# Kernel optimization log

Measured on AMD Instinct MI355X. Metric: run time of the kernel, lower is better.

The kernel has to match this reference:

```python
import jax, jax.numpy as jnp
import numpy as np

S, B, IN, OUT = 16, 32, 1024, 1024


def setup_inputs() -> dict:
    key = jax.random.key(0)
    ks = jax.random.split(key, 7)
    return {
        "input": jax.random.normal(ks[0], (S, B, IN), dtype=jnp.float32),
        "w_mu": jax.random.normal(ks[1], (OUT, IN), dtype=jnp.float32) * 0.1 - 3.0,
        "w_std_eta": jax.random.uniform(ks[2], (OUT, IN), dtype=jnp.float32, minval=-4.0, maxval=-2.0),
        "b_mu": jax.random.normal(ks[3], (OUT,), dtype=jnp.float32) * 0.03,
        "b_std_eta": jax.random.uniform(ks[4], (OUT,), dtype=jnp.float32, minval=-0.03, maxval=0.03),
        "eps_w": jax.random.normal(ks[5], (B, OUT, IN), dtype=jnp.float32),
        "eps_b": jax.random.normal(ks[6], (B, OUT), dtype=jnp.float32),
    }


def _kl_to_std_normal(mu, std):
    # KL( N(mu, std) || N(0, 1) ) elementwise, summed
    return jnp.sum(-jnp.log(std) + 0.5 * (std * std + mu * mu) - 0.5)


def reference(input, w_mu, w_std_eta, b_mu, b_std_eta, eps_w, eps_b):
    std_w = 1e-06 + jax.nn.softplus(w_std_eta)          # [OUT, IN]
    std_b = 1e-06 + jax.nn.softplus(b_std_eta)          # [OUT]
    # per-batch-element reparameterized positive weights: [B, OUT, IN]
    w = jnp.exp(w_mu[None, :, :] + std_w[None, :, :] * eps_w)
    b = b_mu[None, :] + std_b[None, :] * eps_b          # [B, OUT]
    # batched linear: for each b-index i: input[:, i, :] @ w[i].T + b[i]
    out = jnp.einsum('sbi,boi->sbo', input, w) + b[None, :, :]  # [S, B, OUT]
    kl_w = _kl_to_std_normal(w_mu, std_w)
    kl_b = _kl_to_std_normal(b_mu, std_b)
    return (out, kl_w, kl_b)
```

## Files before the change

kernel.cpp:

```cpp
#include <hip/hip_runtime.h>


constexpr int S_ = 16, B_ = 32, IN_ = 1024, OUT_ = 1024;

typedef __bf16 bf16x8 __attribute__((ext_vector_type(8)));
typedef float  f32x4  __attribute__((ext_vector_type(4)));

__device__ __forceinline__ float softplus_f(float x) {
    float e = __expf(-fabsf(x));
    return fmaxf(x, 0.0f) + __logf(1.0f + e);
}

__device__ __forceinline__ unsigned bf16_hi(float x) {
    return (__float_as_uint(x) + 0x8000u) & 0xffff0000u;
}

__global__ __launch_bounds__(256) void bpl_pre2(
    const float* __restrict__ input,
    const float* __restrict__ w_mu, const float* __restrict__ w_eta,
    unsigned* __restrict__ tbl_f,
    __bf16* __restrict__ a_ws,
    float* __restrict__ klw_part)
{
    const int tid = threadIdx.x;

    if (blockIdx.x >= 1024) {
        const int b = blockIdx.x - 1024;
        #pragma unroll
        for (int j = 0; j < 8; ++j) {
            const int c  = tid + j * 256;
            const int k0 = ((c >> 6) << 5) | (((c >> 4) & 3) << 3);
            const int s  = c & 15;
            const float* src = input + ((size_t)s * B_ + b) * IN_ + k0;
            const float4 x0 = *reinterpret_cast<const float4*>(src);
            const float4 x1 = *reinterpret_cast<const float4*>(src + 4);
            bf16x8 v;
            v[0] = (__bf16)x0.x; v[1] = (__bf16)x0.y; v[2] = (__bf16)x0.z; v[3] = (__bf16)x0.w;
            v[4] = (__bf16)x1.x; v[5] = (__bf16)x1.y; v[6] = (__bf16)x1.z; v[7] = (__bf16)x1.w;
            *reinterpret_cast<bf16x8*>(&a_ws[(size_t)b * 16384 + (size_t)c * 8]) = v;
        }
        return;
    }

    __shared__ float red[4];
    const int wid  = tid >> 6;
    const int lane = tid & 63;
    const int o    = blockIdx.x;
    const int ot   = o >> 4;
    const int on   = o & 15;

    const size_t base = (size_t)o * IN_ + tid * 4;
    const float4 mu = *reinterpret_cast<const float4*>(&w_mu[base]);
    const float4 et = *reinterpret_cast<const float4*>(&w_eta[base]);
    const float m[4] = {mu.x, mu.y, mu.z, mu.w};
    const float e[4] = {et.x, et.y, et.z, et.w};

    float local = 0.0f;
    #pragma unroll
    for (int j = 0; j < 4; ++j) {
        const int   i   = tid * 4 + j;
        const float sp  = __logf(1.0f + __expf(e[j])) + 1e-6f;
        const float spl = sp * 1.44269504f;
        const float emu = __expf(m[j]);
        const unsigned pk = bf16_hi(emu) | (bf16_hi(spl) >> 16);
        const int kt  = i >> 5;
        const int kg0 = (i >> 3) & 3;
        const int jj  = i & 7;
        const int ln  = kg0 * 16 + on;
        tbl_f[(((size_t)ot * 32 + kt) * 64 + ln) * 8 + jj] = pk;
        local += -__logf(sp) + 0.5f * fmaf(sp, sp, m[j] * m[j]) - 0.5f;
    }

    #pragma unroll
    for (int off = 32; off > 0; off >>= 1) local += __shfl_xor(local, off, 64);
    if (lane == 0) red[wid] = local;
    __syncthreads();
    if (tid == 0) klw_part[blockIdx.x] = red[0] + red[1] + red[2] + red[3];
}

__global__ __launch_bounds__(512, 4) void bpl_fused(
    const unsigned* __restrict__ tbl_f,
    const __bf16* __restrict__ a_ws,
    const float* __restrict__ eps_w,
    const float* __restrict__ b_mu,
    const float* __restrict__ b_eta,
    const float* __restrict__ eps_b,
    const float* __restrict__ klw_part,
    float* __restrict__ out,
    float* __restrict__ kl)
{
    const int blk = blockIdx.x;
    const int tid = threadIdx.x;

    if (blk == 2048) {
        __shared__ float kred[16];
        const int wid  = tid >> 6;
        const int lane = tid & 63;
        float lw = klw_part[tid] + klw_part[tid + 512];
        float lb;
        {
            const int o = tid;
            const float sd0 = softplus_f(b_eta[o]) + 1e-6f;
            const float m0  = b_mu[o];
            const float sd1 = softplus_f(b_eta[o + 512]) + 1e-6f;
            const float m1  = b_mu[o + 512];
            lb = (-__logf(sd0) + 0.5f * fmaf(sd0, sd0, m0 * m0) - 0.5f)
               + (-__logf(sd1) + 0.5f * fmaf(sd1, sd1, m1 * m1) - 0.5f);
        }
        #pragma unroll
        for (int off = 32; off > 0; off >>= 1) {
            lw += __shfl_xor(lw, off, 64);
            lb += __shfl_xor(lb, off, 64);
        }
        if (lane == 0) { kred[wid] = lw; kred[8 + wid] = lb; }
        __syncthreads();
        if (tid == 0) {
            float tw = 0.0f, tb = 0.0f;
            #pragma unroll
            for (int k = 0; k < 8; ++k) { tw += kred[k]; tb += kred[8 + k]; }
            kl[0] = tw; kl[1] = tb;
        }
        return;
    }

    __shared__ __align__(16) float smem[16384];

    const int xcd = blk & 7;
    const int r_  = blk >> 3;
    const int b   = r_ & 31;
    const int otl = r_ >> 5;
    const int o_base = xcd * 128 + otl * 16;
    const int ot_g   = o_base >> 4;

    const int kq   = tid >> 6;
    const int lane = tid & 63;
    const int on   = lane & 15;
    const int kg0  = lane >> 4;

    const float* eps_base = eps_w + ((size_t)(b * 1024 + o_base)) * 1024 + kq * 128;
    const int rlo = lane >> 5;
    const int cq  = lane & 31;
    float4 ev[8];
    #pragma unroll
    for (int j = 0; j < 8; ++j) {
        const int r = 2 * j + rlo;
        ev[j] = *reinterpret_cast<const float4*>(eps_base + (size_t)r * 1024 + cq * 4);
    }

    const unsigned* tf = tbl_f + (((size_t)ot_g * 32 + kq * 4) * 64 + lane) * 8;
    uint4 t0[4], t1[4];
    #pragma unroll
    for (int t = 0; t < 4; ++t) {
        t0[t] = *reinterpret_cast<const uint4*>(tf + t * 512);
        t1[t] = *reinterpret_cast<const uint4*>(tf + t * 512 + 4);
    }

    const __bf16* ap = a_ws + (size_t)b * 16384 + (size_t)(kq * 4) * 512 + lane * 8;
    bf16x8 av[4];
    #pragma unroll
    for (int t = 0; t < 4; ++t)
        av[t] = *reinterpret_cast<const bf16x8*>(ap + t * 512);

    char* wbase = (char*)(smem + kq * 2048);
    #pragma unroll
    for (int j = 0; j < 8; ++j) {
        const int r    = 2 * j + rlo;
        const int byte = (cq * 16) ^ ((r & 7) << 4);
        *reinterpret_cast<float4*>(wbase + r * 512 + byte) = ev[j];
    }

    f32x4 acc = {0.0f, 0.0f, 0.0f, 0.0f};
    const int sw = (on & 7) << 4;
    #pragma unroll
    for (int t = 0; t < 4; ++t) {
        const f32x4 e0 = *reinterpret_cast<const f32x4*>(
            wbase + on * 512 + ((t * 128 + kg0 * 32) ^ sw));
        const f32x4 e1 = *reinterpret_cast<const f32x4*>(
            wbase + on * 512 + ((t * 128 + kg0 * 32 + 16) ^ sw));

        const unsigned uu[8] = {t0[t].x, t0[t].y, t0[t].z, t0[t].w,
                                t1[t].x, t1[t].y, t1[t].z, t1[t].w};
        const float    ee[8] = {e0[0], e0[1], e0[2], e0[3], e1[0], e1[1], e1[2], e1[3]};

        bf16x8 bfrag;
        #pragma unroll
        for (int q = 0; q < 8; ++q) {
            const float emu = __uint_as_float(uu[q] & 0xffff0000u);
            const float spl = __uint_as_float(uu[q] << 16);
            bfrag[q] = (__bf16)(emu * exp2f(spl * ee[q]));
        }
        acc = __builtin_amdgcn_mfma_f32_16x16x32_bf16(av[t], bfrag, acc, 0, 0, 0);
    }

    *reinterpret_cast<f32x4*>(&smem[kq * 2048 + lane * 4]) = acc;
    __syncthreads();

    if (tid < 256) {
        const int s  = tid >> 4;
        const int ol = tid & 15;
        const int srcLane = ((s >> 2) << 4) | ol;
        const int rr = s & 3;
        float v = 0.0f;
        #pragma unroll
        for (int k8 = 0; k8 < 8; ++k8)
            v += smem[k8 * 2048 + srcLane * 4 + rr];
        const int oo = o_base + ol;
        const float bias = fmaf(softplus_f(b_eta[oo]) + 1e-6f,
                                eps_b[(size_t)b * OUT_ + oo], b_mu[oo]);
        out[((size_t)s * B_ + b) * OUT_ + oo] = v + bias;
    }
}

__global__ __launch_bounds__(256) void bpl_pre_fb(
    const float* __restrict__ w_mu, const float* __restrict__ w_eta,
    const float* __restrict__ b_mu, const float* __restrict__ b_eta,
    float* __restrict__ kl)
{
    __shared__ float red[4];
    const int tid  = threadIdx.x;
    const int wid  = tid >> 6;
    const int lane = tid & 63;

    const size_t base = (size_t)blockIdx.x * IN_ + tid * 4;
    const float4 mu = *reinterpret_cast<const float4*>(&w_mu[base]);
    const float4 et = *reinterpret_cast<const float4*>(&w_eta[base]);
    const float m[4] = {mu.x, mu.y, mu.z, mu.w};
    const float e[4] = {et.x, et.y, et.z, et.w};

    float local = 0.0f;
    #pragma unroll
    for (int j = 0; j < 4; ++j) {
        const float sp = __logf(1.0f + __expf(e[j])) + 1e-6f;
        local += -__logf(sp) + 0.5f * fmaf(sp, sp, m[j] * m[j]) - 0.5f;
    }
    #pragma unroll
    for (int off = 32; off > 0; off >>= 1) local += __shfl_xor(local, off, 64);
    if (lane == 0) red[wid] = local;
    __syncthreads();
    if (tid == 0) atomicAdd(&kl[0], red[0] + red[1] + red[2] + red[3]);

    if (blockIdx.x != 0) return;
    float lb = 0.0f;
    #pragma unroll
    for (int j = 0; j < 4; ++j) {
        const int idx = tid * 4 + j;
        const float sd = softplus_f(b_eta[idx]) + 1e-6f;
        const float mm = b_mu[idx];
        lb += -__logf(sd) + 0.5f * fmaf(sd, sd, mm * mm) - 0.5f;
    }
    #pragma unroll
    for (int off = 32; off > 0; off >>= 1) lb += __shfl_xor(lb, off, 64);
    __syncthreads();
    if (lane == 0) red[wid] = lb;
    __syncthreads();
    if (tid == 0) atomicAdd(&kl[1], red[0] + red[1] + red[2] + red[3]);
}

__global__ __launch_bounds__(256, 4) void bpl_mfma_fb(
    const float* __restrict__ input, const float* __restrict__ w_mu,
    const float* __restrict__ w_eta, const float* __restrict__ b_mu,
    const float* __restrict__ b_eta, const float* __restrict__ eps_w,
    const float* __restrict__ eps_b, float* __restrict__ out)
{
    __shared__ __align__(16) __bf16 alds[16384];

    const int blk = blockIdx.x;
    const int xcd = blk & 7;
    const int r_  = blk >> 3;
    const int b   = r_ & 31;
    const int oh  = r_ >> 5;
    const int o_base = (xcd * 2 + oh) * 64;

    const int tid  = threadIdx.x;
    const int wid  = tid >> 6;
    const int lane = tid & 63;

    #pragma unroll
    for (int j = 0; j < 8; ++j) {
        const int c   = tid + j * 256;
        const int s   = c & 15;
        const int kgg = ((c >> 6) << 2) | ((c >> 4) & 3);
        const float* src = input + ((size_t)s * B_ + b) * IN_ + kgg * 8;
        const float4 x0 = *reinterpret_cast<const float4*>(src);
        const float4 x1 = *reinterpret_cast<const float4*>(src + 4);
        bf16x8 v;
        v[0] = (__bf16)x0.x; v[1] = (__bf16)x0.y; v[2] = (__bf16)x0.z; v[3] = (__bf16)x0.w;
        v[4] = (__bf16)x1.x; v[5] = (__bf16)x1.y; v[6] = (__bf16)x1.z; v[7] = (__bf16)x1.w;
        *reinterpret_cast<bf16x8*>(&alds[c * 8]) = v;
    }
    __syncthreads();

    const int on    = lane & 15;
    const int kg0   = lane >> 4;
    const int o_row = o_base + wid * 16 + on;

    const float* __restrict__ mu_p = w_mu  + (size_t)o_row * IN_ + kg0 * 8;
    const float* __restrict__ et_p = w_eta + (size_t)o_row * IN_ + kg0 * 8;
    const float* __restrict__ ep_p = eps_w + ((size_t)b * OUT_ + o_row) * IN_ + kg0 * 8;
    const __bf16* __restrict__ a_p = alds + lane * 8;

    f32x4 acc = {0.0f, 0.0f, 0.0f, 0.0f};
    #pragma unroll
    for (int kt = 0; kt < 32; ++kt) {
        const int i_ = kt * 32;
        const float4 m0 = *reinterpret_cast<const float4*>(mu_p + i_);
        const float4 m1 = *reinterpret_cast<const float4*>(mu_p + i_ + 4);
        const float4 s0 = *reinterpret_cast<const float4*>(et_p + i_);
        const float4 s1 = *reinterpret_cast<const float4*>(et_p + i_ + 4);
        const float4 e0 = *reinterpret_cast<const float4*>(ep_p + i_);
        const float4 e1 = *reinterpret_cast<const float4*>(ep_p + i_ + 4);
        const float mm[8] = {m0.x, m0.y, m0.z, m0.w, m1.x, m1.y, m1.z, m1.w};
        const float ss[8] = {s0.x, s0.y, s0.z, s0.w, s1.x, s1.y, s1.z, s1.w};
        const float ee[8] = {e0.x, e0.y, e0.z, e0.w, e1.x, e1.y, e1.z, e1.w};
        bf16x8 bfrag;
        #pragma unroll
        for (int q = 0; q < 8; ++q) {
            const float sp_ = __logf(1.0f + __expf(ss[q])) + 1e-6f;
            bfrag[q] = (__bf16)__expf(fmaf(sp_, ee[q], mm[q]));
        }
        const bf16x8 afrag = *reinterpret_cast<const bf16x8*>(a_p + kt * 512);
        acc = __builtin_amdgcn_mfma_f32_16x16x32_bf16(afrag, bfrag, acc, 0, 0, 0);
    }

    const float bias = fmaf(softplus_f(b_eta[o_row]) + 1e-6f,
                            eps_b[(size_t)b * OUT_ + o_row], b_mu[o_row]);
    #pragma unroll
    for (int rr = 0; rr < 4; ++rr) {
        const int s = kg0 * 4 + rr;
        out[((size_t)s * B_ + b) * OUT_ + o_row] = acc[rr] + bias;
    }
}

extern "C" void kernel_launch(void* const* d_in, const int* in_sizes, int n_in,
                              void* d_out, int out_size, void* d_ws, size_t ws_size,
                              hipStream_t stream)
{
    const float* input = (const float*)d_in[0];
    const float* w_mu  = (const float*)d_in[1];
    const float* w_eta = (const float*)d_in[2];
    const float* b_mu  = (const float*)d_in[3];
    const float* b_eta = (const float*)d_in[4];
    const float* eps_w = (const float*)d_in[5];
    const float* eps_b = (const float*)d_in[6];

    float* out = (float*)d_out;
    float* kl  = out + (size_t)S_ * B_ * OUT_;

    const size_t TBL_OFF = 0;
    const size_t A_OFF   = (size_t)4 * 1024 * 1024;
    const size_t KLP_OFF = (size_t)5 * 1024 * 1024;
    const size_t NEED    = KLP_OFF + 4096;

    if (ws_size >= NEED) {
        unsigned* tbl  = (unsigned*)((char*)d_ws + TBL_OFF);
        __bf16*   a_ws = (__bf16*)((char*)d_ws + A_OFF);
        float*    klp  = (float*)((char*)d_ws + KLP_OFF);

        bpl_pre2<<<1056, 256, 0, stream>>>(input, w_mu, w_eta, tbl, a_ws, klp);
        bpl_fused<<<2049, 512, 0, stream>>>(tbl, a_ws, eps_w, b_mu, b_eta, eps_b,
                                            klp, out, kl);
    } else {
        hipMemsetAsync(kl, 0, 2 * sizeof(float), stream);
        bpl_pre_fb<<<1024, 256, 0, stream>>>(w_mu, w_eta, b_mu, b_eta, kl);
        bpl_mfma_fb<<<512, 256, 0, stream>>>(input, w_mu, w_eta, b_mu, b_eta,
                                             eps_w, eps_b, out);
    }
}
```

Measured before the change: 38.43 us.

## Process two batch elements per block to reuse weight table loads

Each fused block now handles two batch indices instead of one, halving the grid from 2049 to 1025 blocks. The per-(o,k) weight table fragment is loaded once and reused for both batches. The second eps_w tile is prefetched into registers while the first is computed, and all 512 threads take part in the final reduction. This cuts table traffic and block launch overhead, at the cost of more registers per thread and fewer blocks to hide the latency of streaming eps_w.

```diff
diff --git a/kernel.cpp b/kernel.cpp
--- a/kernel.cpp
+++ b/kernel.cpp
@@ -92,7 +92,7 @@
     const int blk = blockIdx.x;
     const int tid = threadIdx.x;
 
-    if (blk == 2048) {
+    if (blk == 1024) {
         __shared__ float kred[16];
         const int wid  = tid >> 6;
         const int lane = tid & 63;
@@ -127,8 +127,10 @@
 
     const int xcd = blk & 7;
     const int r_  = blk >> 3;
-    const int b   = r_ & 31;
-    const int otl = r_ >> 5;
+    const int bp  = r_ & 15;
+    const int otl = r_ >> 4;
+    const int b0  = bp * 2;
+    const int b1  = b0 + 1;
     const int o_base = xcd * 128 + otl * 16;
     const int ot_g   = o_base >> 4;
 
@@ -136,16 +138,8 @@
     const int lane = tid & 63;
     const int on   = lane & 15;
     const int kg0  = lane >> 4;
-
-    const float* eps_base = eps_w + ((size_t)(b * 1024 + o_base)) * 1024 + kq * 128;
-    const int rlo = lane >> 5;
-    const int cq  = lane & 31;
-    float4 ev[8];
-    #pragma unroll
-    for (int j = 0; j < 8; ++j) {
-        const int r = 2 * j + rlo;
-        ev[j] = *reinterpret_cast<const float4*>(eps_base + (size_t)r * 1024 + cq * 4);
-    }
+    const int rlo  = lane >> 5;
+    const int cq   = lane & 31;
 
     const unsigned* tf = tbl_f + (((size_t)ot_g * 32 + kq * 4) * 64 + lane) * 8;
     uint4 t0[4], t1[4];
@@ -154,14 +148,23 @@
         t0[t] = *reinterpret_cast<const uint4*>(tf + t * 512);
         t1[t] = *reinterpret_cast<const uint4*>(tf + t * 512 + 4);
     }
-
-    const __bf16* ap = a_ws + (size_t)b * 16384 + (size_t)(kq * 4) * 512 + lane * 8;
-    bf16x8 av[4];
-    #pragma unroll
-    for (int t = 0; t < 4; ++t)
-        av[t] = *reinterpret_cast<const bf16x8*>(ap + t * 512);
-
+    const __bf16* ap0 = a_ws + (size_t)b0 * 16384 + (size_t)(kq * 4) * 512 + lane * 8;
+    const __bf16* ap1 = a_ws + (size_t)b1 * 16384 + (size_t)(kq * 4) * 512 + lane * 8;
+    bf16x8 av0[4], av1[4];
+    #pragma unroll
+    for (int t = 0; t < 4; ++t) {
+        av0[t] = *reinterpret_cast<const bf16x8*>(ap0 + t * 512);
+        av1[t] = *reinterpret_cast<const bf16x8*>(ap1 + t * 512);
+    }
+
+    const float* eb0 = eps_w + ((size_t)(b0 * 1024 + o_base)) * 1024 + kq * 128;
+    const float* eb1 = eps_w + ((size_t)(b1 * 1024 + o_base)) * 1024 + kq * 128;
     char* wbase = (char*)(smem + kq * 2048);
+
+    float4 ev[8];
+    #pragma unroll
+    for (int j = 0; j < 8; ++j)
+        ev[j] = *reinterpret_cast<const float4*>(eb0 + (size_t)(2 * j + rlo) * 1024 + cq * 4);
     #pragma unroll
     for (int j = 0; j < 8; ++j) {
         const int r    = 2 * j + rlo;
@@ -169,19 +172,22 @@
         *reinterpret_cast<float4*>(wbase + r * 512 + byte) = ev[j];
     }
 
-    f32x4 acc = {0.0f, 0.0f, 0.0f, 0.0f};
+    float4 ev1[8];
+    #pragma unroll
+    for (int j = 0; j < 8; ++j)
+        ev1[j] = *reinterpret_cast<const float4*>(eb1 + (size_t)(2 * j + rlo) * 1024 + cq * 4);
+
     const int sw = (on & 7) << 4;
+    f32x4 acc0 = {0.0f, 0.0f, 0.0f, 0.0f};
     #pragma unroll
     for (int t = 0; t < 4; ++t) {
         const f32x4 e0 = *reinterpret_cast<const f32x4*>(
             wbase + on * 512 + ((t * 128 + kg0 * 32) ^ sw));
         const f32x4 e1 = *reinterpret_cast<const f32x4*>(
             wbase + on * 512 + ((t * 128 + kg0 * 32 + 16) ^ sw));
-
         const unsigned uu[8] = {t0[t].x, t0[t].y, t0[t].z, t0[t].w,
                                 t1[t].x, t1[t].y, t1[t].z, t1[t].w};
         const float    ee[8] = {e0[0], e0[1], e0[2], e0[3], e1[0], e1[1], e1[2], e1[3]};
-
         bf16x8 bfrag;
         #pragma unroll
         for (int q = 0; q < 8; ++q) {
@@ -189,25 +195,57 @@
             const float spl = __uint_as_float(uu[q] << 16);
             bfrag[q] = (__bf16)(emu * exp2f(spl * ee[q]));
         }
-        acc = __builtin_amdgcn_mfma_f32_16x16x32_bf16(av[t], bfrag, acc, 0, 0, 0);
-    }
-
-    *reinterpret_cast<f32x4*>(&smem[kq * 2048 + lane * 4]) = acc;
-    __syncthreads();
-
-    if (tid < 256) {
-        const int s  = tid >> 4;
-        const int ol = tid & 15;
+        acc0 = __builtin_amdgcn_mfma_f32_16x16x32_bf16(av0[t], bfrag, acc0, 0, 0, 0);
+    }
+
+    #pragma unroll
+    for (int j = 0; j < 8; ++j) {
+        const int r    = 2 * j + rlo;
+        const int byte = (cq * 16) ^ ((r & 7) << 4);
+        *reinterpret_cast<float4*>(wbase + r * 512 + byte) = ev1[j];
+    }
+
+    f32x4 acc1 = {0.0f, 0.0f, 0.0f, 0.0f};
+    #pragma unroll
+    for (int t = 0; t < 4; ++t) {
+        const f32x4 e0 = *reinterpret_cast<const f32x4*>(
+            wbase + on * 512 + ((t * 128 + kg0 * 32) ^ sw));
+        const f32x4 e1 = *reinterpret_cast<const f32x4*>(
+            wbase + on * 512 + ((t * 128 + kg0 * 32 + 16) ^ sw));
+        const unsigned uu[8] = {t0[t].x, t0[t].y, t0[t].z, t0[t].w,
+                                t1[t].x, t1[t].y, t1[t].z, t1[t].w};
+        const float    ee[8] = {e0[0], e0[1], e0[2], e0[3], e1[0], e1[1], e1[2], e1[3]};
+        bf16x8 bfrag;
+        #pragma unroll
+        for (int q = 0; q < 8; ++q) {
+            const float emu = __uint_as_float(uu[q] & 0xffff0000u);
+            const float spl = __uint_as_float(uu[q] << 16);
+            bfrag[q] = (__bf16)(emu * exp2f(spl * ee[q]));
+        }
+        acc1 = __builtin_amdgcn_mfma_f32_16x16x32_bf16(av1[t], bfrag, acc1, 0, 0, 0);
+    }
+
+    *reinterpret_cast<f32x4*>(&smem[kq * 2048 + lane * 4]) = acc0;
+    *reinterpret_cast<f32x4*>(&smem[kq * 2048 + 1024 + lane * 4]) = acc1;
+    __syncthreads();
+
+    {
+        const int half = tid >> 8;
+        const int t8   = tid & 255;
+        const int s    = t8 >> 4;
+        const int ol   = t8 & 15;
         const int srcLane = ((s >> 2) << 4) | ol;
         const int rr = s & 3;
+        const int off = half * 1024;
         float v = 0.0f;
         #pragma unroll
         for (int k8 = 0; k8 < 8; ++k8)
-            v += smem[k8 * 2048 + srcLane * 4 + rr];
+            v += smem[k8 * 2048 + off + srcLane * 4 + rr];
+        const int bb = half ? b1 : b0;
         const int oo = o_base + ol;
         const float bias = fmaf(softplus_f(b_eta[oo]) + 1e-6f,
-                                eps_b[(size_t)b * OUT_ + oo], b_mu[oo]);
-        out[((size_t)s * B_ + b) * OUT_ + oo] = v + bias;
+                                eps_b[(size_t)bb * OUT_ + oo], b_mu[oo]);
+        out[((size_t)s * B_ + bb) * OUT_ + oo] = v + bias;
     }
 }
 
@@ -357,7 +395,7 @@
         float*    klp  = (float*)((char*)d_ws + KLP_OFF);
 
         bpl_pre2<<<1056, 256, 0, stream>>>(input, w_mu, w_eta, tbl, a_ws, klp);
-        bpl_fused<<<2049, 512, 0, stream>>>(tbl, a_ws, eps_w, b_mu, b_eta, eps_b,
+        bpl_fused<<<1025, 512, 0, stream>>>(tbl, a_ws, eps_w, b_mu, b_eta, eps_b,
                                             klp, out, kl);
     } else {
         hipMemsetAsync(kl, 0, 2 * sizeof(float), stream);
```

Measured after the change: 38.14 us. Within noise of the previous version (-0.8%).
